# Optimization experiments

Measured on AMD Instinct MI355X. Metric: run time of the kernel, lower is better.

Reference implementation:

```python
import jax, jax.numpy as jnp
import numpy as np
import math

CLIP_DIM = 1024
INNER_DIM = 256
NUM_HEADS = 4
HEAD_DIM = INNER_DIM // NUM_HEADS
MASK_BIAS_ALPHA = 5.0
B, N = 16, 1024
LN_EPS = 1e-5


def _layer_norm(x, w, b):
    mu = jnp.mean(x, axis=-1, keepdims=True)
    var = jnp.var(x, axis=-1, keepdims=True)
    return (x - mu) * jax.lax.rsqrt(var + LN_EPS) * w + b


def setup_inputs() -> dict:
    key = jax.random.key(0)
    ks = jax.random.split(key, 12)
    def xavier(k, fan_in, fan_out):
        lim = math.sqrt(6.0 / (fan_in + fan_out))
        return jax.random.uniform(k, (fan_in, fan_out), jnp.float32, -lim, lim)
    return {
        "query_features": jax.random.normal(ks[0], (B, N, CLIP_DIM), jnp.float32),
        "support_features": jax.random.normal(ks[1], (B, N, CLIP_DIM), jnp.float32),
        "support_mask_weights": jax.random.uniform(ks[2], (B, N), jnp.float32),
        "ln_q_w": jnp.ones((CLIP_DIM,), jnp.float32),
        "ln_q_b": jnp.zeros((CLIP_DIM,), jnp.float32),
        "ln_s_w": jnp.ones((CLIP_DIM,), jnp.float32),
        "ln_s_b": jnp.zeros((CLIP_DIM,), jnp.float32),
        "Wq": xavier(ks[3], CLIP_DIM, INNER_DIM), "bq": jnp.zeros((INNER_DIM,), jnp.float32),
        "Wk": xavier(ks[4], CLIP_DIM, INNER_DIM), "bk": jnp.zeros((INNER_DIM,), jnp.float32),
        "Wv": xavier(ks[5], CLIP_DIM, INNER_DIM), "bv": jnp.zeros((INNER_DIM,), jnp.float32),
        "Wo": xavier(ks[6], INNER_DIM, CLIP_DIM), "bo": jnp.zeros((CLIP_DIM,), jnp.float32),
        "Wg": xavier(ks[7], CLIP_DIM, CLIP_DIM), "bg": jnp.full((CLIP_DIM,), -2.0, jnp.float32),
    }


def reference(query_features, support_features, support_mask_weights,
              ln_q_w, ln_q_b, ln_s_w, ln_s_b,
              Wq, bq, Wk, bk, Wv, bv, Wo, bo, Wg, bg):
    b, n, _ = query_features.shape
    q = _layer_norm(query_features, ln_q_w, ln_q_b)
    s = _layer_norm(support_features, ln_s_w, ln_s_b)
    # project and split heads: (B, H, N, D)
    Q = (q @ Wq + bq).reshape(b, n, NUM_HEADS, HEAD_DIM).transpose(0, 2, 1, 3)
    K = (s @ Wk + bk).reshape(b, n, NUM_HEADS, HEAD_DIM).transpose(0, 2, 1, 3)
    V = (s @ Wv + bv).reshape(b, n, NUM_HEADS, HEAD_DIM).transpose(0, 2, 1, 3)
    logits = jnp.einsum("bhqd,bhkd->bhqk", Q, K) / math.sqrt(HEAD_DIM)
    logits = logits + (MASK_BIAS_ALPHA * support_mask_weights)[:, None, None, :]
    attn = jax.nn.softmax(logits, axis=-1)
    context = jnp.einsum("bhqk,bhkd->bhqd", attn, V)
    context = context.transpose(0, 2, 1, 3).reshape(b, n, INNER_DIM)
    cross = context @ Wo + bo
    gate = jax.nn.sigmoid(query_features @ Wg + bg)
    enhanced = query_features + gate * cross
    return enhanced, attn
```

## Files before the change

kernel.cpp:

```cpp
#include <hip/hip_runtime.h>
#include <hip/hip_bf16.h>
#include <math.h>

typedef __attribute__((ext_vector_type(8))) short bf16x8;
typedef __attribute__((ext_vector_type(4))) float f32x4;
typedef __hip_bfloat16 bf16;

#define MFMA16(a, b, c) __builtin_amdgcn_mfma_f32_16x16x32_bf16((a), (b), (c), 0, 0, 0)

__device__ inline float redmax16(float v) {
    v = fmaxf(v, __shfl_xor(v, 1));
    v = fmaxf(v, __shfl_xor(v, 2));
    v = fmaxf(v, __shfl_xor(v, 4));
    v = fmaxf(v, __shfl_xor(v, 8));
    return v;
}
__device__ inline float redsum16(float v) {
    v += __shfl_xor(v, 1);
    v += __shfl_xor(v, 2);
    v += __shfl_xor(v, 4);
    v += __shfl_xor(v, 8);
    return v;
}

__global__ void transpose_cast(const float* __restrict__ src, bf16* __restrict__ dst,
                               int K, int N, int total) {
    int i = blockIdx.x * 256 + threadIdx.x;
    if (i >= total) return;
    int n = i / K, k = i - n * K;
    dst[i] = __float2bfloat16(src[(size_t)k * N + n]);
}

union Pack4 { bf16 h[4]; uint2 v; };

__global__ __launch_bounds__(256) void ln_kernel(
    const float* __restrict__ qf, const float* __restrict__ sf,
    const float* __restrict__ qw, const float* __restrict__ qb,
    const float* __restrict__ sw, const float* __restrict__ sb,
    bf16* __restrict__ qn, bf16* __restrict__ sn, bf16* __restrict__ qraw) {
    int row = blockIdx.x;
    bool isQ = row < 16384;
    int r = isQ ? row : row - 16384;
    const float* src = (isQ ? qf : sf) + (size_t)r * 1024;
    const float* w = isQ ? qw : sw;
    const float* b = isQ ? qb : sb;
    int t = threadIdx.x;
    float4 x = reinterpret_cast<const float4*>(src)[t];
    float s = x.x + x.y + x.z + x.w;
    float ss = x.x * x.x + x.y * x.y + x.z * x.z + x.w * x.w;
    #pragma unroll
    for (int m = 1; m < 64; m <<= 1) { s += __shfl_xor(s, m); ss += __shfl_xor(ss, m); }
    __shared__ float rs_[4], rss_[4];
    int wave = t >> 6;
    if ((t & 63) == 0) { rs_[wave] = s; rss_[wave] = ss; }
    __syncthreads();
    s = rs_[0] + rs_[1] + rs_[2] + rs_[3];
    ss = rss_[0] + rss_[1] + rss_[2] + rss_[3];
    float mu = s * (1.0f / 1024.0f);
    float var = ss * (1.0f / 1024.0f) - mu * mu;
    float rstd = rsqrtf(var + 1e-5f);
    float4 wv = reinterpret_cast<const float4*>(w)[t];
    float4 bv = reinterpret_cast<const float4*>(b)[t];
    Pack4 o;
    o.h[0] = __float2bfloat16((x.x - mu) * rstd * wv.x + bv.x);
    o.h[1] = __float2bfloat16((x.y - mu) * rstd * wv.y + bv.y);
    o.h[2] = __float2bfloat16((x.z - mu) * rstd * wv.z + bv.z);
    o.h[3] = __float2bfloat16((x.w - mu) * rstd * wv.w + bv.w);
    bf16* dst = (isQ ? qn : sn) + (size_t)r * 1024 + t * 4;
    *reinterpret_cast<uint2*>(dst) = o.v;
    if (isQ) {
        Pack4 o2;
        o2.h[0] = __float2bfloat16(x.x);
        o2.h[1] = __float2bfloat16(x.y);
        o2.h[2] = __float2bfloat16(x.z);
        o2.h[3] = __float2bfloat16(x.w);
        bf16* d2 = qraw + (size_t)r * 1024 + t * 4;
        *reinterpret_cast<uint2*>(d2) = o2.v;
    }
}

template <int MODE>
__global__ __launch_bounds__(256) void gemm_bf16(
    const bf16* __restrict__ A, const bf16* __restrict__ Bt,
    const float* __restrict__ bias, void* __restrict__ outp,
    const bf16* __restrict__ gate, const float* __restrict__ resid,
    int M, int N, int Kd) {
    __shared__ short lsA[128 * 72];
    __shared__ short lsB[128 * 72];
    int tid = threadIdx.x;
    int m0 = blockIdx.x * 128, n0 = blockIdx.y * 128;
    int wave = tid >> 6, lane = tid & 63;
    int wr = wave >> 1, wc = wave & 1;
    int lrow = lane & 15, kgrp = lane >> 4;
    f32x4 acc[4][4];
    #pragma unroll
    for (int i = 0; i < 4; i++)
        #pragma unroll
        for (int j = 0; j < 4; j++) acc[i][j] = (f32x4){0.f, 0.f, 0.f, 0.f};
    int nkt = Kd >> 6;
    for (int kt = 0; kt < nkt; kt++) {
        int k0 = kt * 64;
        #pragma unroll
        for (int i = 0; i < 4; i++) {
            int ci = tid + i * 256;
            int row = ci >> 3, cc = ci & 7;
            *reinterpret_cast<bf16x8*>(lsA + row * 72 + cc * 8) =
                *reinterpret_cast<const bf16x8*>(A + (size_t)(m0 + row) * Kd + k0 + cc * 8);
            *reinterpret_cast<bf16x8*>(lsB + row * 72 + cc * 8) =
                *reinterpret_cast<const bf16x8*>(Bt + (size_t)(n0 + row) * Kd + k0 + cc * 8);
        }
        __syncthreads();
        #pragma unroll
        for (int kc = 0; kc < 2; kc++) {
            bf16x8 aF[4], bF[4];
            #pragma unroll
            for (int mf = 0; mf < 4; mf++)
                aF[mf] = *reinterpret_cast<const bf16x8*>(
                    lsA + (wr * 64 + mf * 16 + lrow) * 72 + kc * 32 + kgrp * 8);
            #pragma unroll
            for (int nf = 0; nf < 4; nf++)
                bF[nf] = *reinterpret_cast<const bf16x8*>(
                    lsB + (wc * 64 + nf * 16 + lrow) * 72 + kc * 32 + kgrp * 8);
            #pragma unroll
            for (int mf = 0; mf < 4; mf++)
                #pragma unroll
                for (int nf = 0; nf < 4; nf++)
                    acc[mf][nf] = MFMA16(aF[mf], bF[nf], acc[mf][nf]);
        }
        __syncthreads();
    }
    #pragma unroll
    for (int mf = 0; mf < 4; mf++) {
        #pragma unroll
        for (int nf = 0; nf < 4; nf++) {
            #pragma unroll
            for (int r = 0; r < 4; r++) {
                int gM = m0 + wr * 64 + mf * 16 + kgrp * 4 + r;
                int gN = n0 + wc * 64 + nf * 16 + lrow;
                float v = acc[mf][nf][r] + bias[gN];
                if (MODE == 0) {
                    int b = gM >> 10, n = gM & 1023, h = gN >> 6, d = gN & 63;
                    ((bf16*)outp)[(((size_t)(b * 4 + h)) << 16) + (n << 6) + d] = __float2bfloat16(v);
                } else if (MODE == 1) {
                    int b = gM >> 10, n = gM & 1023, h = gN >> 6, d = gN & 63;
                    ((bf16*)outp)[(((size_t)(b * 4 + h)) << 16) + (d << 10) + n] = __float2bfloat16(v);
                } else if (MODE == 2) {
                    float g = 1.0f / (1.0f + __expf(-v));
                    ((bf16*)outp)[(size_t)gM * N + gN] = __float2bfloat16(g);
                } else {
                    float g = __bfloat162float(gate[(size_t)gM * N + gN]);
                    float q = resid[(size_t)gM * N + gN];
                    ((float*)outp)[(size_t)gM * N + gN] = q + g * v;
                }
            }
        }
    }
}

__global__ __launch_bounds__(256) void attn_kernel(
    const bf16* __restrict__ Qh, const bf16* __restrict__ Kh, const bf16* __restrict__ Vt,
    const float* __restrict__ mask, float* __restrict__ attn_out, bf16* __restrict__ ctx) {
    __shared__ bf16 Plds[4 * 16 * 32];
    int bh = blockIdx.x >> 4, qt = blockIdx.x & 15;
    int b = bh >> 2, h = bh & 3;
    int wave = threadIdx.x >> 6, lane = threadIdx.x & 63;
    int lrow = lane & 15, kgrp = lane >> 4;
    const bf16* Qb = Qh + ((size_t)bh << 16);
    const bf16* Kb = Kh + ((size_t)bh << 16);
    const bf16* Vb = Vt + ((size_t)bh << 16);
    const float* mb = mask + b * 1024;
    int q0 = qt * 64 + wave * 16;
    bf16x8 aQ0 = *reinterpret_cast<const bf16x8*>(Qb + (q0 + lrow) * 64 + kgrp * 8);
    bf16x8 aQ1 = *reinterpret_cast<const bf16x8*>(Qb + (q0 + lrow) * 64 + 32 + kgrp * 8);
    float mrun[4], ssum[4];
    #pragma unroll
    for (int r = 0; r < 4; r++) { mrun[r] = -1e30f; ssum[r] = 0.f; }
    for (int kt = 0; kt < 64; kt++) {
        bf16x8 bK0 = *reinterpret_cast<const bf16x8*>(Kb + (kt * 16 + lrow) * 64 + kgrp * 8);
        bf16x8 bK1 = *reinterpret_cast<const bf16x8*>(Kb + (kt * 16 + lrow) * 64 + 32 + kgrp * 8);
        f32x4 acc = (f32x4){0.f, 0.f, 0.f, 0.f};
        acc = MFMA16(aQ0, bK0, acc);
        acc = MFMA16(aQ1, bK1, acc);
        float mv = 5.0f * mb[kt * 16 + lrow];
        #pragma unroll
        for (int r = 0; r < 4; r++) {
            float s = acc[r] * 0.125f + mv;
            float tm = redmax16(s);
            float nm = fmaxf(mrun[r], tm);
            float e = __expf(s - nm);
            float es = redsum16(e);
            ssum[r] = ssum[r] * __expf(mrun[r] - nm) + es;
            mrun[r] = nm;
        }
    }
    float inv[4];
    #pragma unroll
    for (int r = 0; r < 4; r++) inv[r] = 1.0f / ssum[r];
    f32x4 cacc[4];
    #pragma unroll
    for (int nf = 0; nf < 4; nf++) cacc[nf] = (f32x4){0.f, 0.f, 0.f, 0.f};
    float* aout = attn_out + ((size_t)bh << 20) + (size_t)q0 * 1024;
    for (int kt = 0; kt < 64; kt++) {
        bf16x8 bK0 = *reinterpret_cast<const bf16x8*>(Kb + (kt * 16 + lrow) * 64 + kgrp * 8);
        bf16x8 bK1 = *reinterpret_cast<const bf16x8*>(Kb + (kt * 16 + lrow) * 64 + 32 + kgrp * 8);
        f32x4 acc = (f32x4){0.f, 0.f, 0.f, 0.f};
        acc = MFMA16(aQ0, bK0, acc);
        acc = MFMA16(aQ1, bK1, acc);
        float mv = 5.0f * mb[kt * 16 + lrow];
        #pragma unroll
        for (int r = 0; r < 4; r++) {
            float s = acc[r] * 0.125f + mv;
            float p = __expf(s - mrun[r]) * inv[r];
            aout[(kgrp * 4 + r) * 1024 + kt * 16 + lrow] = p;
            Plds[wave * 512 + (kgrp * 4 + r) * 32 + ((kt & 1) << 4) + lrow] = __float2bfloat16(p);
        }
        if (kt & 1) {
            __syncthreads();
            bf16x8 aP = *reinterpret_cast<const bf16x8*>(&Plds[wave * 512 + lrow * 32 + kgrp * 8]);
            int k2 = (kt >> 1) * 32;
            #pragma unroll
            for (int nf = 0; nf < 4; nf++) {
                bf16x8 bV = *reinterpret_cast<const bf16x8*>(Vb + (nf * 16 + lrow) * 1024 + k2 + kgrp * 8);
                cacc[nf] = MFMA16(aP, bV, cacc[nf]);
            }
            __syncthreads();
        }
    }
    #pragma unroll
    for (int nf = 0; nf < 4; nf++) {
        #pragma unroll
        for (int r = 0; r < 4; r++) {
            int qrow = q0 + kgrp * 4 + r;
            ctx[((size_t)(b * 1024 + qrow)) * 256 + h * 64 + nf * 16 + lrow] =
                __float2bfloat16(cacc[nf][r]);
        }
    }
}

extern "C" void kernel_launch(void* const* d_in, const int* in_sizes, int n_in,
                              void* d_out, int out_size, void* d_ws, size_t ws_size,
                              hipStream_t stream) {
    const float* qf = (const float*)d_in[0];
    const float* sf = (const float*)d_in[1];
    const float* mask = (const float*)d_in[2];
    const float* lnqw = (const float*)d_in[3];
    const float* lnqb = (const float*)d_in[4];
    const float* lnsw = (const float*)d_in[5];
    const float* lnsb = (const float*)d_in[6];
    const float* Wq = (const float*)d_in[7];
    const float* bq = (const float*)d_in[8];
    const float* Wk = (const float*)d_in[9];
    const float* bk = (const float*)d_in[10];
    const float* Wv = (const float*)d_in[11];
    const float* bv = (const float*)d_in[12];
    const float* Wo = (const float*)d_in[13];
    const float* bo = (const float*)d_in[14];
    const float* Wg = (const float*)d_in[15];
    const float* bg = (const float*)d_in[16];

    char* ws = (char*)d_ws;
    const size_t MB = 1024 * 1024;
    bf16* wqt  = (bf16*)(ws + 0);
    bf16* wkt  = (bf16*)(ws + 512 * 1024);
    bf16* wvt  = (bf16*)(ws + 1024 * 1024);
    bf16* wot  = (bf16*)(ws + 1536 * 1024);
    bf16* wgt  = (bf16*)(ws + 2 * MB);
    bf16* qn   = (bf16*)(ws + 4 * MB);
    bf16* sn   = (bf16*)(ws + 36 * MB);
    bf16* qraw = (bf16*)(ws + 68 * MB);
    bf16* Qh   = (bf16*)(ws + 100 * MB);
    bf16* Kh   = (bf16*)(ws + 108 * MB);
    bf16* Vt   = (bf16*)(ws + 116 * MB);
    bf16* gate = qn;
    bf16* ctx  = sn;

    float* enh = (float*)d_out;
    float* attn = enh + (size_t)16 * 1024 * 1024;

    transpose_cast<<<1024, 256, 0, stream>>>(Wq, wqt, 1024, 256, 262144);
    transpose_cast<<<1024, 256, 0, stream>>>(Wk, wkt, 1024, 256, 262144);
    transpose_cast<<<1024, 256, 0, stream>>>(Wv, wvt, 1024, 256, 262144);
    transpose_cast<<<1024, 256, 0, stream>>>(Wo, wot, 256, 1024, 262144);
    transpose_cast<<<4096, 256, 0, stream>>>(Wg, wgt, 1024, 1024, 1048576);
    ln_kernel<<<32768, 256, 0, stream>>>(qf, sf, lnqw, lnqb, lnsw, lnsb, qn, sn, qraw);
    gemm_bf16<0><<<dim3(128, 2), 256, 0, stream>>>(qn, wqt, bq, Qh, nullptr, nullptr, 16384, 256, 1024);
    gemm_bf16<0><<<dim3(128, 2), 256, 0, stream>>>(sn, wkt, bk, Kh, nullptr, nullptr, 16384, 256, 1024);
    gemm_bf16<1><<<dim3(128, 2), 256, 0, stream>>>(sn, wvt, bv, Vt, nullptr, nullptr, 16384, 256, 1024);
    attn_kernel<<<1024, 256, 0, stream>>>(Qh, Kh, Vt, mask, attn, ctx);
    gemm_bf16<2><<<dim3(128, 8), 256, 0, stream>>>(qraw, wgt, bg, gate, nullptr, nullptr, 16384, 1024, 1024);
    gemm_bf16<3><<<dim3(128, 8), 256, 0, stream>>>(ctx, wot, bo, enh, gate, qf, 16384, 1024, 256);
}
```

Baseline: 832.2 us.

## Fuse K/V projection, shrink QKV tiles, restructure attention softmax passes, tile weight transpose

```diff
diff --git a/kernel.cpp b/kernel.cpp
--- a/kernel.cpp
+++ b/kernel.cpp
@@ -8,27 +8,23 @@
 
 #define MFMA16(a, b, c) __builtin_amdgcn_mfma_f32_16x16x32_bf16((a), (b), (c), 0, 0, 0)
 
-__device__ inline float redmax16(float v) {
-    v = fmaxf(v, __shfl_xor(v, 1));
-    v = fmaxf(v, __shfl_xor(v, 2));
-    v = fmaxf(v, __shfl_xor(v, 4));
-    v = fmaxf(v, __shfl_xor(v, 8));
-    return v;
-}
-__device__ inline float redsum16(float v) {
-    v += __shfl_xor(v, 1);
-    v += __shfl_xor(v, 2);
-    v += __shfl_xor(v, 4);
-    v += __shfl_xor(v, 8);
-    return v;
-}
-
-__global__ void transpose_cast(const float* __restrict__ src, bf16* __restrict__ dst,
-                               int K, int N, int total) {
-    int i = blockIdx.x * 256 + threadIdx.x;
-    if (i >= total) return;
-    int n = i / K, k = i - n * K;
-    dst[i] = __float2bfloat16(src[(size_t)k * N + n]);
+static __device__ inline short f2bf(float f) {
+    bf16 h = __float2bfloat16(f);
+    return *reinterpret_cast<short*>(&h);
+}
+
+__global__ __launch_bounds__(256) void transpose_cast(const float* __restrict__ src,
+                                                      bf16* __restrict__ dst, int K, int N) {
+    __shared__ float t[32][33];
+    int n0 = blockIdx.x * 32, k0 = blockIdx.y * 32;
+    int tx = threadIdx.x & 31, ty = threadIdx.x >> 5;
+    #pragma unroll
+    for (int j = 0; j < 4; j++)
+        t[ty + 8 * j][tx] = src[(size_t)(k0 + ty + 8 * j) * N + n0 + tx];
+    __syncthreads();
+    #pragma unroll
+    for (int j = 0; j < 4; j++)
+        dst[(size_t)(n0 + ty + 8 * j) * K + k0 + tx] = __float2bfloat16(t[tx][ty + 8 * j]);
 }
 
 union Pack4 { bf16 h[4]; uint2 v; };
@@ -79,50 +75,56 @@
     }
 }
 
-template <int MODE>
+template <int MODE, int BM>
 __global__ __launch_bounds__(256) void gemm_bf16(
     const bf16* __restrict__ A, const bf16* __restrict__ Bt,
-    const float* __restrict__ bias, void* __restrict__ outp,
+    const float* __restrict__ bias, const float* __restrict__ bias2,
+    void* __restrict__ outp, void* __restrict__ outp2,
     const bf16* __restrict__ gate, const float* __restrict__ resid,
     int M, int N, int Kd) {
-    __shared__ short lsA[128 * 72];
-    __shared__ short lsB[128 * 72];
+    constexpr int MF = BM / 32;
+    __shared__ alignas(16) short lsA[BM * 72];
+    __shared__ alignas(16) short lsB[128 * 72];
     int tid = threadIdx.x;
-    int m0 = blockIdx.x * 128, n0 = blockIdx.y * 128;
+    int m0 = blockIdx.x * BM, n0 = blockIdx.y * 128;
     int wave = tid >> 6, lane = tid & 63;
     int wr = wave >> 1, wc = wave & 1;
     int lrow = lane & 15, kgrp = lane >> 4;
-    f32x4 acc[4][4];
-    #pragma unroll
-    for (int i = 0; i < 4; i++)
+    f32x4 acc[MF][4];
+    #pragma unroll
+    for (int i = 0; i < MF; i++)
         #pragma unroll
         for (int j = 0; j < 4; j++) acc[i][j] = (f32x4){0.f, 0.f, 0.f, 0.f};
     int nkt = Kd >> 6;
     for (int kt = 0; kt < nkt; kt++) {
         int k0 = kt * 64;
-        #pragma unroll
-        for (int i = 0; i < 4; i++) {
-            int ci = tid + i * 256;
-            int row = ci >> 3, cc = ci & 7;
+        constexpr int CA = BM * 8 / 256;
+        #pragma unroll
+        for (int i = 0; i < CA; i++) {
+            int ci = tid + i * 256, row = ci >> 3, cc = ci & 7;
             *reinterpret_cast<bf16x8*>(lsA + row * 72 + cc * 8) =
                 *reinterpret_cast<const bf16x8*>(A + (size_t)(m0 + row) * Kd + k0 + cc * 8);
+        }
+        #pragma unroll
+        for (int i = 0; i < 4; i++) {
+            int ci = tid + i * 256, row = ci >> 3, cc = ci & 7;
             *reinterpret_cast<bf16x8*>(lsB + row * 72 + cc * 8) =
                 *reinterpret_cast<const bf16x8*>(Bt + (size_t)(n0 + row) * Kd + k0 + cc * 8);
         }
         __syncthreads();
         #pragma unroll
         for (int kc = 0; kc < 2; kc++) {
-            bf16x8 aF[4], bF[4];
-            #pragma unroll
-            for (int mf = 0; mf < 4; mf++)
+            bf16x8 aF[MF], bF[4];
+            #pragma unroll
+            for (int mf = 0; mf < MF; mf++)
                 aF[mf] = *reinterpret_cast<const bf16x8*>(
-                    lsA + (wr * 64 + mf * 16 + lrow) * 72 + kc * 32 + kgrp * 8);
+                    lsA + (wr * (BM / 2) + mf * 16 + lrow) * 72 + kc * 32 + kgrp * 8);
             #pragma unroll
             for (int nf = 0; nf < 4; nf++)
                 bF[nf] = *reinterpret_cast<const bf16x8*>(
                     lsB + (wc * 64 + nf * 16 + lrow) * 72 + kc * 32 + kgrp * 8);
             #pragma unroll
-            for (int mf = 0; mf < 4; mf++)
+            for (int mf = 0; mf < MF; mf++)
                 #pragma unroll
                 for (int nf = 0; nf < 4; nf++)
                     acc[mf][nf] = MFMA16(aF[mf], bF[nf], acc[mf][nf]);
@@ -130,24 +132,34 @@
         __syncthreads();
     }
     #pragma unroll
-    for (int mf = 0; mf < 4; mf++) {
+    for (int mf = 0; mf < MF; mf++) {
         #pragma unroll
         for (int nf = 0; nf < 4; nf++) {
             #pragma unroll
             for (int r = 0; r < 4; r++) {
-                int gM = m0 + wr * 64 + mf * 16 + kgrp * 4 + r;
+                int gM = m0 + wr * (BM / 2) + mf * 16 + kgrp * 4 + r;
                 int gN = n0 + wc * 64 + nf * 16 + lrow;
-                float v = acc[mf][nf][r] + bias[gN];
                 if (MODE == 0) {
+                    float v = acc[mf][nf][r] + bias[gN];
                     int b = gM >> 10, n = gM & 1023, h = gN >> 6, d = gN & 63;
                     ((bf16*)outp)[(((size_t)(b * 4 + h)) << 16) + (n << 6) + d] = __float2bfloat16(v);
-                } else if (MODE == 1) {
-                    int b = gM >> 10, n = gM & 1023, h = gN >> 6, d = gN & 63;
-                    ((bf16*)outp)[(((size_t)(b * 4 + h)) << 16) + (d << 10) + n] = __float2bfloat16(v);
+                } else if (MODE == 4) {
+                    int b = gM >> 10, n = gM & 1023;
+                    if (gN < 256) {
+                        float v = acc[mf][nf][r] + bias[gN];
+                        int h = gN >> 6, d = gN & 63;
+                        ((bf16*)outp)[(((size_t)(b * 4 + h)) << 16) + (n << 6) + d] = __float2bfloat16(v);
+                    } else {
+                        float v = acc[mf][nf][r] + bias2[gN - 256];
+                        int h = (gN - 256) >> 6, d = gN & 63;
+                        ((bf16*)outp2)[(((size_t)(b * 4 + h)) << 16) + (d << 10) + n] = __float2bfloat16(v);
+                    }
                 } else if (MODE == 2) {
+                    float v = acc[mf][nf][r] + bias[gN];
                     float g = 1.0f / (1.0f + __expf(-v));
                     ((bf16*)outp)[(size_t)gM * N + gN] = __float2bfloat16(g);
                 } else {
+                    float v = acc[mf][nf][r] + bias[gN];
                     float g = __bfloat162float(gate[(size_t)gM * N + gN]);
                     float q = resid[(size_t)gM * N + gN];
                     ((float*)outp)[(size_t)gM * N + gN] = q + g * v;
@@ -160,7 +172,8 @@
 __global__ __launch_bounds__(256) void attn_kernel(
     const bf16* __restrict__ Qh, const bf16* __restrict__ Kh, const bf16* __restrict__ Vt,
     const float* __restrict__ mask, float* __restrict__ attn_out, bf16* __restrict__ ctx) {
-    __shared__ bf16 Plds[4 * 16 * 32];
+    __shared__ alignas(16) short P2[4][2][16][40];
+    __shared__ float ms_[4][16], is_[4][16];
     int bh = blockIdx.x >> 4, qt = blockIdx.x & 15;
     int b = bh >> 2, h = bh & 3;
     int wave = threadIdx.x >> 6, lane = threadIdx.x & 63;
@@ -170,69 +183,83 @@
     const bf16* Vb = Vt + ((size_t)bh << 16);
     const float* mb = mask + b * 1024;
     int q0 = qt * 64 + wave * 16;
-    bf16x8 aQ0 = *reinterpret_cast<const bf16x8*>(Qb + (q0 + lrow) * 64 + kgrp * 8);
-    bf16x8 aQ1 = *reinterpret_cast<const bf16x8*>(Qb + (q0 + lrow) * 64 + 32 + kgrp * 8);
-    float mrun[4], ssum[4];
-    #pragma unroll
-    for (int r = 0; r < 4; r++) { mrun[r] = -1e30f; ssum[r] = 0.f; }
+    bf16x8 qf0 = *reinterpret_cast<const bf16x8*>(Qb + (q0 + lrow) * 64 + kgrp * 8);
+    bf16x8 qf1 = *reinterpret_cast<const bf16x8*>(Qb + (q0 + lrow) * 64 + 32 + kgrp * 8);
+
+    float mx = -1e30f;
     for (int kt = 0; kt < 64; kt++) {
-        bf16x8 bK0 = *reinterpret_cast<const bf16x8*>(Kb + (kt * 16 + lrow) * 64 + kgrp * 8);
-        bf16x8 bK1 = *reinterpret_cast<const bf16x8*>(Kb + (kt * 16 + lrow) * 64 + 32 + kgrp * 8);
+        bf16x8 kf0 = *reinterpret_cast<const bf16x8*>(Kb + (kt * 16 + lrow) * 64 + kgrp * 8);
+        bf16x8 kf1 = *reinterpret_cast<const bf16x8*>(Kb + (kt * 16 + lrow) * 64 + 32 + kgrp * 8);
         f32x4 acc = (f32x4){0.f, 0.f, 0.f, 0.f};
-        acc = MFMA16(aQ0, bK0, acc);
-        acc = MFMA16(aQ1, bK1, acc);
-        float mv = 5.0f * mb[kt * 16 + lrow];
-        #pragma unroll
-        for (int r = 0; r < 4; r++) {
-            float s = acc[r] * 0.125f + mv;
-            float tm = redmax16(s);
-            float nm = fmaxf(mrun[r], tm);
-            float e = __expf(s - nm);
-            float es = redsum16(e);
-            ssum[r] = ssum[r] * __expf(mrun[r] - nm) + es;
-            mrun[r] = nm;
-        }
-    }
-    float inv[4];
-    #pragma unroll
-    for (int r = 0; r < 4; r++) inv[r] = 1.0f / ssum[r];
+        acc = MFMA16(kf0, qf0, acc);
+        acc = MFMA16(kf1, qf1, acc);
+        float4 mv = *reinterpret_cast<const float4*>(mb + kt * 16 + kgrp * 4);
+        float s0 = fmaxf(acc[0] * 0.125f + 5.f * mv.x, acc[1] * 0.125f + 5.f * mv.y);
+        float s1 = fmaxf(acc[2] * 0.125f + 5.f * mv.z, acc[3] * 0.125f + 5.f * mv.w);
+        mx = fmaxf(mx, fmaxf(s0, s1));
+    }
+    mx = fmaxf(mx, __shfl_xor(mx, 16));
+    mx = fmaxf(mx, __shfl_xor(mx, 32));
+
+    float ssum = 0.f;
     f32x4 cacc[4];
     #pragma unroll
     for (int nf = 0; nf < 4; nf++) cacc[nf] = (f32x4){0.f, 0.f, 0.f, 0.f};
-    float* aout = attn_out + ((size_t)bh << 20) + (size_t)q0 * 1024;
     for (int kt = 0; kt < 64; kt++) {
-        bf16x8 bK0 = *reinterpret_cast<const bf16x8*>(Kb + (kt * 16 + lrow) * 64 + kgrp * 8);
-        bf16x8 bK1 = *reinterpret_cast<const bf16x8*>(Kb + (kt * 16 + lrow) * 64 + 32 + kgrp * 8);
+        bf16x8 kf0 = *reinterpret_cast<const bf16x8*>(Kb + (kt * 16 + lrow) * 64 + kgrp * 8);
+        bf16x8 kf1 = *reinterpret_cast<const bf16x8*>(Kb + (kt * 16 + lrow) * 64 + 32 + kgrp * 8);
         f32x4 acc = (f32x4){0.f, 0.f, 0.f, 0.f};
-        acc = MFMA16(aQ0, bK0, acc);
-        acc = MFMA16(aQ1, bK1, acc);
-        float mv = 5.0f * mb[kt * 16 + lrow];
-        #pragma unroll
-        for (int r = 0; r < 4; r++) {
-            float s = acc[r] * 0.125f + mv;
-            float p = __expf(s - mrun[r]) * inv[r];
-            aout[(kgrp * 4 + r) * 1024 + kt * 16 + lrow] = p;
-            Plds[wave * 512 + (kgrp * 4 + r) * 32 + ((kt & 1) << 4) + lrow] = __float2bfloat16(p);
-        }
+        acc = MFMA16(kf0, qf0, acc);
+        acc = MFMA16(kf1, qf1, acc);
+        float4 mv = *reinterpret_cast<const float4*>(mb + kt * 16 + kgrp * 4);
+        float e0 = __expf(acc[0] * 0.125f + 5.f * mv.x - mx);
+        float e1 = __expf(acc[1] * 0.125f + 5.f * mv.y - mx);
+        float e2 = __expf(acc[2] * 0.125f + 5.f * mv.z - mx);
+        float e3 = __expf(acc[3] * 0.125f + 5.f * mv.w - mx);
+        ssum += (e0 + e1) + (e2 + e3);
+        short4 pk;
+        pk.x = f2bf(e0); pk.y = f2bf(e1); pk.z = f2bf(e2); pk.w = f2bf(e3);
+        *reinterpret_cast<short4*>(&P2[wave][(kt >> 1) & 1][lrow][(kt & 1) * 16 + kgrp * 4]) = pk;
         if (kt & 1) {
             __syncthreads();
-            bf16x8 aP = *reinterpret_cast<const bf16x8*>(&Plds[wave * 512 + lrow * 32 + kgrp * 8]);
+            bf16x8 aP = *reinterpret_cast<const bf16x8*>(&P2[wave][(kt >> 1) & 1][lrow][kgrp * 8]);
             int k2 = (kt >> 1) * 32;
             #pragma unroll
             for (int nf = 0; nf < 4; nf++) {
                 bf16x8 bV = *reinterpret_cast<const bf16x8*>(Vb + (nf * 16 + lrow) * 1024 + k2 + kgrp * 8);
                 cacc[nf] = MFMA16(aP, bV, cacc[nf]);
             }
-            __syncthreads();
-        }
-    }
+        }
+    }
+    ssum += __shfl_xor(ssum, 16);
+    ssum += __shfl_xor(ssum, 32);
+    float inv = 1.0f / ssum;
+    if (kgrp == 0) { ms_[wave][lrow] = mx; is_[wave][lrow] = inv; }
+    __syncthreads();
+    float m4[4], i4[4];
+    #pragma unroll
+    for (int r = 0; r < 4; r++) { m4[r] = ms_[wave][kgrp * 4 + r]; i4[r] = is_[wave][kgrp * 4 + r]; }
     #pragma unroll
     for (int nf = 0; nf < 4; nf++) {
         #pragma unroll
         for (int r = 0; r < 4; r++) {
             int qrow = q0 + kgrp * 4 + r;
             ctx[((size_t)(b * 1024 + qrow)) * 256 + h * 64 + nf * 16 + lrow] =
-                __float2bfloat16(cacc[nf][r]);
+                __float2bfloat16(cacc[nf][r] * i4[r]);
+        }
+    }
+    float* aout = attn_out + ((size_t)bh << 20) + (size_t)q0 * 1024;
+    for (int kt = 0; kt < 64; kt++) {
+        bf16x8 kf0 = *reinterpret_cast<const bf16x8*>(Kb + (kt * 16 + lrow) * 64 + kgrp * 8);
+        bf16x8 kf1 = *reinterpret_cast<const bf16x8*>(Kb + (kt * 16 + lrow) * 64 + 32 + kgrp * 8);
+        f32x4 acc = (f32x4){0.f, 0.f, 0.f, 0.f};
+        acc = MFMA16(qf0, kf0, acc);
+        acc = MFMA16(qf1, kf1, acc);
+        float mv = 5.f * mb[kt * 16 + lrow];
+        #pragma unroll
+        for (int r = 0; r < 4; r++) {
+            float p = __expf(acc[r] * 0.125f + mv - m4[r]) * i4[r];
+            aout[(kgrp * 4 + r) * 1024 + kt * 16 + lrow] = p;
         }
     }
 }
@@ -277,16 +304,19 @@
     float* enh = (float*)d_out;
     float* attn = enh + (size_t)16 * 1024 * 1024;
 
-    transpose_cast<<<1024, 256, 0, stream>>>(Wq, wqt, 1024, 256, 262144);
-    transpose_cast<<<1024, 256, 0, stream>>>(Wk, wkt, 1024, 256, 262144);
-    transpose_cast<<<1024, 256, 0, stream>>>(Wv, wvt, 1024, 256, 262144);
-    transpose_cast<<<1024, 256, 0, stream>>>(Wo, wot, 256, 1024, 262144);
-    transpose_cast<<<4096, 256, 0, stream>>>(Wg, wgt, 1024, 1024, 1048576);
+    transpose_cast<<<dim3(8, 32), 256, 0, stream>>>(Wq, wqt, 1024, 256);
+    transpose_cast<<<dim3(8, 32), 256, 0, stream>>>(Wk, wkt, 1024, 256);
+    transpose_cast<<<dim3(8, 32), 256, 0, stream>>>(Wv, wvt, 1024, 256);
+    transpose_cast<<<dim3(32, 8), 256, 0, stream>>>(Wo, wot, 256, 1024);
+    transpose_cast<<<dim3(32, 32), 256, 0, stream>>>(Wg, wgt, 1024, 1024);
     ln_kernel<<<32768, 256, 0, stream>>>(qf, sf, lnqw, lnqb, lnsw, lnsb, qn, sn, qraw);
-    gemm_bf16<0><<<dim3(128, 2), 256, 0, stream>>>(qn, wqt, bq, Qh, nullptr, nullptr, 16384, 256, 1024);
-    gemm_bf16<0><<<dim3(128, 2), 256, 0, stream>>>(sn, wkt, bk, Kh, nullptr, nullptr, 16384, 256, 1024);
-    gemm_bf16<1><<<dim3(128, 2), 256, 0, stream>>>(sn, wvt, bv, Vt, nullptr, nullptr, 16384, 256, 1024);
+    gemm_bf16<0, 64><<<dim3(256, 2), 256, 0, stream>>>(qn, wqt, bq, nullptr, Qh, nullptr,
+                                                       nullptr, nullptr, 16384, 256, 1024);
+    gemm_bf16<4, 64><<<dim3(256, 4), 256, 0, stream>>>(sn, wkt, bk, bv, Kh, Vt,
+                                                       nullptr, nullptr, 16384, 512, 1024);
     attn_kernel<<<1024, 256, 0, stream>>>(Qh, Kh, Vt, mask, attn, ctx);
-    gemm_bf16<2><<<dim3(128, 8), 256, 0, stream>>>(qraw, wgt, bg, gate, nullptr, nullptr, 16384, 1024, 1024);
-    gemm_bf16<3><<<dim3(128, 8), 256, 0, stream>>>(ctx, wot, bo, enh, gate, qf, 16384, 1024, 256);
-}
+    gemm_bf16<2, 128><<<dim3(128, 8), 256, 0, stream>>>(qraw, wgt, bg, nullptr, gate, nullptr,
+                                                        nullptr, nullptr, 16384, 1024, 1024);
+    gemm_bf16<3, 128><<<dim3(128, 8), 256, 0, stream>>>(ctx, wot, bo, nullptr, enh, nullptr,
+                                                        gate, qf, 16384, 1024, 256);
+}
```

New measurement: 866.8 us. 1.04x slower.
